# Performance work log

Hardware: AMD Instinct MI355X
Metric: run time of the kernel (lower is better)

Reference implementation:

```python
import jax, jax.numpy as jnp
import numpy as np


def _bilinear_gather(corr, x, y):
    # corr: [N, H2, W2]; x, y: [N, K, K] pixel coords; zero padding outside,
    # matching F.grid_sample(mode='bilinear', padding_mode='zeros', align_corners=True).
    N, H2, W2 = corr.shape
    corr_flat = corr.reshape(N, H2 * W2)
    x0 = jnp.floor(x)
    y0 = jnp.floor(y)
    wx1 = x - x0
    wy1 = y - y0

    def gather(xi, yi):
        valid = (xi >= 0) & (xi <= W2 - 1) & (yi >= 0) & (yi <= H2 - 1)
        xc = jnp.clip(xi, 0, W2 - 1).astype(jnp.int32)
        yc = jnp.clip(yi, 0, H2 - 1).astype(jnp.int32)
        idx = (yc * W2 + xc).reshape(N, -1)
        vals = jnp.take_along_axis(corr_flat, idx, axis=1).reshape(xi.shape)
        return jnp.where(valid, vals, jnp.zeros((), corr.dtype))

    return (gather(x0, y0) * (1 - wx1) * (1 - wy1)
            + gather(x0 + 1, y0) * wx1 * (1 - wy1)
            + gather(x0, y0 + 1) * (1 - wx1) * wy1
            + gather(x0 + 1, y0 + 1) * wx1 * wy1)


def setup_inputs() -> dict:
    key = jax.random.key(0)
    k1, k2, k3 = jax.random.split(key, 3)
    B, D, H, W = 2, 256, 64, 64
    fmap1 = jax.random.normal(k1, (B, D, H, W), dtype=jnp.float32)
    fmap2 = jax.random.normal(k2, (B, D, H, W), dtype=jnp.float32)
    # coords in pixel space [0, W-1]
    coords = jax.random.uniform(k3, (B, 2, H, W), dtype=jnp.float32) * (W - 1)
    return {"fmap1": fmap1, "fmap2": fmap2, "coords": coords, "radius": 4}


def reference(fmap1, fmap2, coords, radius):
    B, D, H, W = fmap1.shape
    # all-pairs correlation: [B, H*W, H*W], scaled by 1/sqrt(D)
    f1 = fmap1.reshape(B, D, H * W)
    f2 = fmap2.reshape(B, D, H * W)
    corr = jnp.einsum('bdn,bdm->bnm', f1, f2) / jnp.sqrt(jnp.asarray(D, jnp.float32))
    corr = corr.reshape(B * H * W, H, W)

    r = radius
    K = 2 * r + 1
    d = jnp.linspace(-r, r, K, dtype=jnp.float32)
    dyg, dxg = jnp.meshgrid(d, d, indexing='ij')
    delta = jnp.stack([dyg, dxg], axis=-1)  # [K, K, 2] (matches torch.meshgrid(dy, dx))

    centroid = coords.transpose(0, 2, 3, 1).reshape(B * H * W, 1, 1, 2)
    coords_lvl = centroid + delta[None]  # [N, K, K, 2]
    # RAFT bilinear_sampler: channel 0 is x, channel 1 is y
    x = coords_lvl[..., 0]
    y = coords_lvl[..., 1]

    out = _bilinear_gather(corr, x, y)  # [N, K, K]
    out = out.reshape(B, H, W, K * K).transpose(0, 3, 1, 2)
    return out.astype(jnp.float32)
```

## Files before the change

### kernel.cpp

```cpp
#include <hip/hip_runtime.h>

#define HWC 4096
#define WC 64
#define HC 64
#define DC 256
#define BC 2
#define KKC 81

typedef _Float16 h2 __attribute__((ext_vector_type(2)));
typedef _Float16 h8 __attribute__((ext_vector_type(8)));

static __device__ inline float dot8(h8 v, h8 a, float s) {
#if __has_builtin(__builtin_amdgcn_fdot2)
    s = __builtin_amdgcn_fdot2((h2){v[0], v[1]}, (h2){a[0], a[1]}, s, false);
    s = __builtin_amdgcn_fdot2((h2){v[2], v[3]}, (h2){a[2], a[3]}, s, false);
    s = __builtin_amdgcn_fdot2((h2){v[4], v[5]}, (h2){a[4], a[5]}, s, false);
    s = __builtin_amdgcn_fdot2((h2){v[6], v[7]}, (h2){a[6], a[7]}, s, false);
#else
#pragma unroll
    for (int k = 0; k < 8; ++k) s += (float)v[k] * (float)a[k];
#endif
    return s;
}

__global__ __launch_bounds__(256) void transpose_h_k(const float* __restrict__ f1,
                                                     const float* __restrict__ f2,
                                                     _Float16* __restrict__ o1,
                                                     _Float16* __restrict__ o2) {
    __shared__ float tile[64][33];
    const int z = blockIdx.z;
    const int b = z & 1;
    const float* in = (z >> 1) ? f2 : f1;
    _Float16* out = (z >> 1) ? o2 : o1;
    in += (size_t)b * DC * HWC;
    out += (size_t)b * HWC * DC;

    const int m0 = blockIdx.x * 32, d0 = blockIdx.y * 64;
    const int tx = threadIdx.x, ty = threadIdx.y;
#pragma unroll
    for (int k = 0; k < 8; ++k) {
        const int d = d0 + ty + k * 8;
        tile[ty + k * 8][tx] = in[(size_t)d * HWC + m0 + tx];
    }
    __syncthreads();
#pragma unroll
    for (int k = 0; k < 4; ++k) {
        const int ml = ty + k * 8;
        const int m = m0 + ml;
        h2 h = {(_Float16)tile[2 * tx][ml], (_Float16)tile[2 * tx + 1][ml]};
        ((h2*)(out + (size_t)m * DC + d0))[tx] = h;
    }
}

__global__ __launch_bounds__(256) void corr_k(const _Float16* __restrict__ f1t,
                                              const _Float16* __restrict__ f2t,
                                              const float* __restrict__ coords,
                                              float* __restrict__ out) {
    __shared__ float Cs[100];

    const int bid = blockIdx.x;
    const int xcd = bid & 7;
    const int b = xcd >> 2;
    const int hw = ((bid >> 3) << 2) + (xcd & 3);

    const int tid = threadIdx.x;
    const int g = tid >> 4;
    const int l = tid & 15;

    const float x = coords[((size_t)b * 2 + 0) * HWC + hw];
    const float y = coords[((size_t)b * 2 + 1) * HWC + hw];
    const float x0f = floorf(x), y0f = floorf(y);
    const float wx = x - x0f, wy = y - y0f;
    const int ix0 = (int)x0f, iy0 = (int)y0f;

    const h8* ap = (const h8*)(f1t) + ((size_t)(b * HWC + hw)) * 32 + l * 2;
    const h8 a0 = ap[0], a1 = ap[1];
    const h8* f2b = (const h8*)(f2t) + (size_t)b * HWC * 32;

#pragma unroll
    for (int it = 0; it < 7; ++it) {
        const int t = it * 16 + g;
        if (t < 100) {
            const int yi = t / 10, xi = t - yi * 10;
            const int gy = iy0 - 4 + yi, gx = ix0 - 4 + xi;
            float s = 0.f;
            if (gx >= 0 && gx < WC && gy >= 0 && gy < HC) {
                const h8* vp = f2b + (size_t)(gy * WC + gx) * 32 + l * 2;
                const h8 v0 = vp[0], v1 = vp[1];
                s = dot8(v0, a0, s);
                s = dot8(v1, a1, s);
            }
            s += __shfl_xor(s, 1, 64);
            s += __shfl_xor(s, 2, 64);
            s += __shfl_xor(s, 4, 64);
            s += __shfl_xor(s, 8, 64);
            if (l == 0) Cs[t] = s * 0.0625f;
        }
    }
    __syncthreads();

    if (tid < KKC) {
        const int i = tid / 9, j = tid % 9;
        const float w00 = (1.f - wx) * (1.f - wy);
        const float w01 = wx * (1.f - wy);
        const float w10 = (1.f - wx) * wy;
        const float w11 = wx * wy;
        const float r = w00 * Cs[j * 10 + i]       + w01 * Cs[j * 10 + i + 1] +
                        w10 * Cs[(j + 1) * 10 + i] + w11 * Cs[(j + 1) * 10 + i + 1];
        out[((size_t)(b * KKC + tid)) * HWC + hw] = r;
    }
}

extern "C" void kernel_launch(void* const* d_in, const int* in_sizes, int n_in,
                              void* d_out, int out_size, void* d_ws, size_t ws_size,
                              hipStream_t stream) {
    const float* fmap1 = (const float*)d_in[0];
    const float* fmap2 = (const float*)d_in[1];
    const float* coords = (const float*)d_in[2];
    float* out = (float*)d_out;

    const size_t perH = (size_t)BC * HWC * DC;
    _Float16* f1t = (_Float16*)d_ws;
    _Float16* f2t = f1t + perH;

    transpose_h_k<<<dim3(HWC / 32, DC / 64, 4), dim3(32, 8), 0, stream>>>(fmap1, fmap2, f1t, f2t);
    corr_k<<<dim3(BC * HWC), dim3(256), 0, stream>>>(f1t, f2t, coords, out);
}
```

Before: 91.75 us.

## Drop fmap1 transpose, load f1 column in corr kernel, use DPP reductions

Only fmap2 is transposed to fp16 now. Each corr block gathers its own fmap1 column directly from the original layout into shared memory, which removes half the transpose traffic and its workspace writes. The transpose writes 16-byte vectors, and the correlation loop clamps indices so loads are branch-free. The warp-shuffle reductions become DPP adds. In exchange, the strided fmap1 gather in corr_k is uncoalesced, and an extra sync is added per block.

New measurement: 96.70 us. +5.4%, slower.

```diff
diff --git a/kernel.cpp b/kernel.cpp
--- a/kernel.cpp
+++ b/kernel.cpp
@@ -23,40 +23,37 @@
     return s;
 }
 
-__global__ __launch_bounds__(256) void transpose_h_k(const float* __restrict__ f1,
-                                                     const float* __restrict__ f2,
-                                                     _Float16* __restrict__ o1,
-                                                     _Float16* __restrict__ o2) {
+#define DPP_ADD(x, ctrl) \
+    ((x) + __int_as_float(__builtin_amdgcn_update_dpp(0, __float_as_int(x), (ctrl), 0xF, 0xF, true)))
+
+__global__ __launch_bounds__(256) void transpose_h_k(const float* __restrict__ in0,
+                                                     _Float16* __restrict__ out0) {
     __shared__ float tile[64][33];
-    const int z = blockIdx.z;
-    const int b = z & 1;
-    const float* in = (z >> 1) ? f2 : f1;
-    _Float16* out = (z >> 1) ? o2 : o1;
-    in += (size_t)b * DC * HWC;
-    out += (size_t)b * HWC * DC;
+    const int b = blockIdx.z;
+    const float* in = in0 + (size_t)b * DC * HWC;
+    _Float16* out = out0 + (size_t)b * HWC * DC;
+    const int m0 = blockIdx.x * 32, d0 = blockIdx.y * 64;
+    const int tid = threadIdx.x;
 
-    const int m0 = blockIdx.x * 32, d0 = blockIdx.y * 64;
-    const int tx = threadIdx.x, ty = threadIdx.y;
+    const int tx = tid & 31, ty = tid >> 5;
 #pragma unroll
-    for (int k = 0; k < 8; ++k) {
-        const int d = d0 + ty + k * 8;
-        tile[ty + k * 8][tx] = in[(size_t)d * HWC + m0 + tx];
-    }
+    for (int k = 0; k < 8; ++k)
+        tile[ty + k * 8][tx] = in[(size_t)(d0 + ty + k * 8) * HWC + m0 + tx];
     __syncthreads();
+
+    const int dx = tid & 7, my = tid >> 3;
+    h8 v;
 #pragma unroll
-    for (int k = 0; k < 4; ++k) {
-        const int ml = ty + k * 8;
-        const int m = m0 + ml;
-        h2 h = {(_Float16)tile[2 * tx][ml], (_Float16)tile[2 * tx + 1][ml]};
-        ((h2*)(out + (size_t)m * DC + d0))[tx] = h;
-    }
+    for (int e = 0; e < 8; ++e) v[e] = (_Float16)tile[dx * 8 + e][my];
+    *(h8*)(out + (size_t)(m0 + my) * DC + d0 + dx * 8) = v;
 }
 
-__global__ __launch_bounds__(256) void corr_k(const _Float16* __restrict__ f1t,
+__global__ __launch_bounds__(256) void corr_k(const float* __restrict__ f1,
                                               const _Float16* __restrict__ f2t,
                                               const float* __restrict__ coords,
                                               float* __restrict__ out) {
-    __shared__ float Cs[100];
+    __shared__ float Cs[112];
+    __shared__ float f1s[DC];
 
     const int bid = blockIdx.x;
     const int xcd = bid & 7;
@@ -67,35 +64,41 @@
     const int g = tid >> 4;
     const int l = tid & 15;
 
+    f1s[tid] = f1[((size_t)b * DC + tid) * HWC + hw];
+
     const float x = coords[((size_t)b * 2 + 0) * HWC + hw];
     const float y = coords[((size_t)b * 2 + 1) * HWC + hw];
     const float x0f = floorf(x), y0f = floorf(y);
     const float wx = x - x0f, wy = y - y0f;
     const int ix0 = (int)x0f, iy0 = (int)y0f;
+    __syncthreads();
 
-    const h8* ap = (const h8*)(f1t) + ((size_t)(b * HWC + hw)) * 32 + l * 2;
-    const h8 a0 = ap[0], a1 = ap[1];
-    const h8* f2b = (const h8*)(f2t) + (size_t)b * HWC * 32;
+    const float* fp = f1s + l * 16;
+    h8 a0, a1;
+#pragma unroll
+    for (int e = 0; e < 8; ++e) { a0[e] = (_Float16)fp[e]; a1[e] = (_Float16)fp[8 + e]; }
+
+    const h8* f2b = (const h8*)f2t + (size_t)b * HWC * 32;
 
 #pragma unroll
     for (int it = 0; it < 7; ++it) {
         const int t = it * 16 + g;
-        if (t < 100) {
-            const int yi = t / 10, xi = t - yi * 10;
-            const int gy = iy0 - 4 + yi, gx = ix0 - 4 + xi;
-            float s = 0.f;
-            if (gx >= 0 && gx < WC && gy >= 0 && gy < HC) {
-                const h8* vp = f2b + (size_t)(gy * WC + gx) * 32 + l * 2;
-                const h8 v0 = vp[0], v1 = vp[1];
-                s = dot8(v0, a0, s);
-                s = dot8(v1, a1, s);
-            }
-            s += __shfl_xor(s, 1, 64);
-            s += __shfl_xor(s, 2, 64);
-            s += __shfl_xor(s, 4, 64);
-            s += __shfl_xor(s, 8, 64);
-            if (l == 0) Cs[t] = s * 0.0625f;
-        }
+        const int yi = t / 10, xi = t - yi * 10;
+        const int gy = iy0 - 4 + yi, gx = ix0 - 4 + xi;
+        const int gyc = min(max(gy, 0), HC - 1);
+        const int gxc = min(max(gx, 0), WC - 1);
+        const bool valid = ((unsigned)gy < (unsigned)HC) &
+                           ((unsigned)gx < (unsigned)WC) & (t < 100);
+        const h8* vp = f2b + (size_t)(gyc * WC + gxc) * 32 + l * 2;
+        const h8 v0 = vp[0], v1 = vp[1];
+        float s = dot8(v0, a0, 0.f);
+        s = dot8(v1, a1, s);
+        s = valid ? s : 0.f;
+        s = DPP_ADD(s, 0xB1);
+        s = DPP_ADD(s, 0x4E);
+        s = DPP_ADD(s, 0x124);
+        s = DPP_ADD(s, 0x128);
+        if (l == 0) Cs[t] = s * 0.0625f;
     }
     __syncthreads();
 
@@ -119,10 +122,8 @@
     const float* coords = (const float*)d_in[2];
     float* out = (float*)d_out;
 
-    const size_t perH = (size_t)BC * HWC * DC;
-    _Float16* f1t = (_Float16*)d_ws;
-    _Float16* f2t = f1t + perH;
+    _Float16* f2t = (_Float16*)d_ws;
 
-    transpose_h_k<<<dim3(HWC / 32, DC / 64, 4), dim3(32, 8), 0, stream>>>(fmap1, fmap2, f1t, f2t);
-    corr_k<<<dim3(BC * HWC), dim3(256), 0, stream>>>(f1t, f2t, coords, out);
+    transpose_h_k<<<dim3(HWC / 32, DC / 64, BC), dim3(256), 0, stream>>>(fmap2, f2t);
+    corr_k<<<dim3(BC * HWC), dim3(256), 0, stream>>>(fmap1, f2t, coords, out);
 }
```
